# Optimization experiments

Hardware: AMD Instinct MI355X
Metric: run time of the kernel (lower is better)

## Reference

```python
import jax, jax.numpy as jnp
import numpy as np

B, K, LQ, LR, H = 32, 8, 128, 256, 512  # H = hidden_dim*2
L = LQ + K * LR


def setup_inputs() -> dict:
    key = jax.random.key(0)
    ks = jax.random.split(key, 10)
    w = 0.02
    return {
        "h_q": jax.random.normal(ks[0], (B, LQ, H), jnp.float32),
        "q_mask": jnp.ones((B, LQ), jnp.float32),
        "h_r": jax.random.normal(ks[1], (B, K, LR, H), jnp.float32),
        "r_mask": jnp.ones((B, K, LR), jnp.float32),
        "s_t": jax.random.normal(ks[2], (B, H), jnp.float32),
        "qr_cov": jnp.zeros((B, L), jnp.float32),
        # Linear weights stored torch-style [out, in]
        "U_w": jax.random.normal(ks[3], (H, H), jnp.float32) * w,
        "Wc_w": jax.random.normal(ks[4], (H, 1), jnp.float32) * w,
        "Ws_w": jax.random.normal(ks[5], (H, H), jnp.float32) * w,
        "Wqr_w": jax.random.normal(ks[6], (H, H), jnp.float32) * w,
        "Wqr_b": jax.random.normal(ks[7], (H,), jnp.float32) * w,
        "Vr_w": jax.random.normal(ks[8], (1, H), jnp.float32) * w,
    }


def reference(h_q, q_mask, h_r, r_mask, s_t, qr_cov,
              U_w, Wc_w, Ws_w, Wqr_w, Wqr_b, Vr_w):
    b, l_q, h = h_q.shape
    _, k, l_r, _ = h_r.shape

    _h_q = jnp.broadcast_to(h_q[:, None], (b, k, l_q, h)).reshape(b * k, l_q, h)
    _h_r = h_r.reshape(b * k, l_r, h)
    _q_mask = jnp.broadcast_to(q_mask[:, None], (b, k, l_q)).reshape(b * k, l_q)
    _r_mask = r_mask.reshape(b * k, l_r)

    # bilinear co-attention scores: tanh((hq @ U^T) @ hr^T)  [b*k, l_q, l_r]
    hqU = jnp.einsum('bqi,oi->bqo', _h_q, U_w)
    U = jnp.tanh(jnp.einsum('bqo,bro->bqr', hqU, _h_r))

    alpha_q = jax.nn.softmax(jnp.max(U, axis=2), axis=-1)  # [b*k, l_q]
    alpha_r = jax.nn.softmax(jnp.max(U, axis=1), axis=-1)  # [b*k, l_r]

    pai_q = ((alpha_q * _q_mask)[..., None] * _h_q).reshape(b, k, l_q, h).mean(axis=1)
    pai_r = ((alpha_r * _r_mask)[..., None] * _h_r).reshape(b, k * l_r, h)
    qr = jnp.concatenate([pai_q, pai_r], axis=1)  # [b, L, h]

    dec_fea = (jnp.einsum('bi,oi->bo', s_t, Ws_w)[:, None, :]
               + jnp.einsum('bli,oi->blo', qr, Wqr_w) + Wqr_b
               + qr_cov[:, :, None] * Wc_w[:, 0])  # coverage feature

    logits = jnp.einsum('blo,o->bl', jnp.tanh(dec_fea), Vr_w[0])  # [b, L]
    mask = jnp.concatenate([q_mask, r_mask.reshape(b, k * l_r)], axis=1)
    a = jax.nn.softmax(logits, axis=1) * mask
    a = a / jnp.sum(a, axis=1, keepdims=True)

    c_t = jnp.einsum('bl,blh->bh', a, qr)
    new_cov = qr_cov + a
    return (c_t, a, new_cov)
```

## Files before the change

kernel.cpp:

```cpp
#include <hip/hip_runtime.h>
#include <stdint.h>

#define B  32
#define KK 8
#define LQ 128
#define LR 256
#define H  512
#define LL 2176

typedef short s16x8 __attribute__((ext_vector_type(8)));
typedef float f32x4 __attribute__((ext_vector_type(4)));

__device__ __forceinline__ unsigned short f2bf(float f) {
    unsigned int u = __float_as_uint(f);
    unsigned int r = (u + 0x7FFFu + ((u >> 16) & 1u)) >> 16;
    return (unsigned short)r;
}
__device__ __forceinline__ void gload16(const unsigned short* g, unsigned short* l) {
    __builtin_amdgcn_global_load_lds(
        (const __attribute__((address_space(1))) void*)g,
        (__attribute__((address_space(3))) void*)l, 16, 0, 0);
}
__device__ __forceinline__ float fexp2(float x) {
#if __has_builtin(__builtin_amdgcn_exp2f)
    return __builtin_amdgcn_exp2f(x);
#else
    return __expf(x * 0.69314718056f);
#endif
}
__device__ __forceinline__ float frcp(float x) {
#if __has_builtin(__builtin_amdgcn_rcpf)
    return __builtin_amdgcn_rcpf(x);
#else
    return 1.f / x;
#endif
}
__device__ __forceinline__ float fast_tanh(float x) {
    float e = fexp2(x * 2.885390082f);
    return 1.f - 2.f * frcp(1.f + e);
}
#define LOG2E 1.4426950408889634f

#define NQ4 (B * LQ * H / 4)
#define NR4 (B * KK * LR * H / 4)
#define NW4 (H * H / 4)
#define NL4 (B * LL / 4)
#define NC4 (B * H / 4)
#define NWB4 (B * LL / 4)
#define QBLK 256
#define RBLK 4096
#define WBLK 64
#define ZBLK 19
#define SBLK 256
#define K0GRID (QBLK + RBLK + WBLK + ZBLK + SBLK)
__global__ __launch_bounds__(256) void k0_convert(
    const float* __restrict__ h_q, const float* __restrict__ h_r,
    const float* __restrict__ U_w, const float* __restrict__ Wqr_w,
    unsigned short* __restrict__ Xb, unsigned short* __restrict__ Uwb,
    unsigned short* __restrict__ Wqrb, float* __restrict__ logits,
    float* __restrict__ out_ct, float* __restrict__ wbuf,
    const float* __restrict__ s_t, const float* __restrict__ Ws_w,
    float* __restrict__ sWs) {
    int t = threadIdx.x;
    int blk = blockIdx.x;
    ushort4* Xb4 = (ushort4*)Xb;
    if (blk < QBLK + RBLK) {
        const float4* src; ushort4* dst;
        if (blk < QBLK) {
            unsigned u0 = (unsigned)blk * 2048u;
            unsigned b = (unsigned)blk >> 3;
            src = (const float4*)h_q + u0;
            dst = Xb4 + b * 278528u + (u0 & 16383u);
        } else {
            unsigned rb = (unsigned)(blk - QBLK);
            unsigned u0 = rb * 2048u;
            unsigned b = rb >> 7;
            src = (const float4*)h_r + u0;
            dst = Xb4 + b * 278528u + 16384u + (u0 & 262143u);
        }
        float4 v[8];
#pragma unroll
        for (int j = 0; j < 8; ++j) v[j] = src[t + j * 256];
#pragma unroll
        for (int j = 0; j < 8; ++j) {
            ushort4 o;
            o.x = f2bf(v[j].x); o.y = f2bf(v[j].y);
            o.z = f2bf(v[j].z); o.w = f2bf(v[j].w);
            dst[t + j * 256] = o;
        }
    } else if (blk < QBLK + RBLK + WBLK) {
        int wb = blk - (QBLK + RBLK);
        const float4* src = ((wb < 32) ? (const float4*)U_w : (const float4*)Wqr_w)
                            + (unsigned)(wb & 31) * 2048u;
        ushort4* dst = ((wb < 32) ? (ushort4*)Uwb : (ushort4*)Wqrb)
                       + (unsigned)(wb & 31) * 2048u;
        float4 v[8];
#pragma unroll
        for (int j = 0; j < 8; ++j) v[j] = src[t + j * 256];
#pragma unroll
        for (int j = 0; j < 8; ++j) {
            ushort4 o;
            o.x = f2bf(v[j].x); o.y = f2bf(v[j].y);
            o.z = f2bf(v[j].z); o.w = f2bf(v[j].w);
            dst[t + j * 256] = o;
        }
    } else if (blk < QBLK + RBLK + WBLK + ZBLK) {
        unsigned zb = (unsigned)(blk - (QBLK + RBLK + WBLK));
        float4 zero = {0.f, 0.f, 0.f, 0.f};
        float4* lg4 = (float4*)logits;
        float4* ct4 = (float4*)out_ct;
        float4* wb4 = (float4*)wbuf;
#pragma unroll
        for (int j = 0; j < 8; ++j) {
            unsigned z = zb * 2048u + (unsigned)j * 256u + (unsigned)t;
            if (z < NL4) lg4[z] = zero;
            else if (z < NL4 + NC4) ct4[z - NL4] = zero;
            else if (z < NL4 + NC4 + NWB4) wb4[z - NL4 - NC4] = zero;
        }
    } else {
        int idx = blk - (QBLK + RBLK + WBLK + ZBLK);
        int b = idx >> 3, oc = idx & 7;
        __shared__ __align__(16) float sl[H];
        for (int i = t; i < H; i += 256) sl[i] = s_t[b * H + i];
        __syncthreads();
        int o = oc * 64 + (t >> 2);
        int part = t & 3;
        const float4* sl4 = (const float4*)sl;
        const float4* wr4 = (const float4*)(Ws_w + (size_t)o * H);
        float a = 0.f;
#pragma unroll
        for (int ii = 0; ii < 32; ++ii) {
            int i = part + 4 * ii;
            float4 x = sl4[i], y = wr4[i];
            a += x.x * y.x + x.y * y.y + x.z * y.z + x.w * y.w;
        }
        a += __shfl_xor(a, 1);
        a += __shfl_xor(a, 2);
        if (part == 0) sWs[b * H + o] = a;
    }
}

__global__ __launch_bounds__(256) void k1_gemm_hqU(
    const unsigned short* __restrict__ Xb, const unsigned short* __restrict__ Uwb,
    unsigned short* __restrict__ hqU) {
    __shared__ __align__(16) unsigned short As[64 * 64];
    __shared__ __align__(16) unsigned short Bs[128 * 64];
    int tid = threadIdx.x;
    int wave = tid >> 6, lane = tid & 63;
    int quad = lane >> 4, l16 = lane & 15;
    int wr = wave >> 1, wc = wave & 1;
    int g = blockIdx.x;
    int tle = (g & 7) * 32 + (g >> 3);
    int mt = tle >> 2, nt = tle & 3;
    int m0 = mt * 64, n0 = nt * 128;

    const unsigned short* ag[2]; unsigned short* la[2];
    const unsigned short* bg[4]; unsigned short* lb[4];
#pragma unroll
    for (int i = 0; i < 2; ++i) {
        int gg = (wave * 2 + i) * 64 + lane;
        int r = gg >> 3, c = gg & 7, cs = c ^ (r & 7);
        int am = m0 + r;
        ag[i] = Xb + ((size_t)(am >> 7) * LL + (am & 127)) * H + cs * 8;
        la[i] = As + (wave * 2 + i) * 512;
    }
#pragma unroll
    for (int i = 0; i < 4; ++i) {
        int gg = (wave * 4 + i) * 64 + lane;
        int r = gg >> 3, c = gg & 7, cs = c ^ (r & 7);
        bg[i] = Uwb + (size_t)(n0 + r) * H + cs * 8;
        lb[i] = Bs + (wave * 4 + i) * 512;
    }

    f32x4 acc[2][4] = {};
    for (int k0 = 0; k0 < H; k0 += 64) {
#pragma unroll
        for (int i = 0; i < 2; ++i) gload16(ag[i] + k0, la[i]);
#pragma unroll
        for (int i = 0; i < 4; ++i) gload16(bg[i] + k0, lb[i]);
        __syncthreads();
#pragma unroll
        for (int kh = 0; kh < 2; ++kh) {
            s16x8 af[2], bfr[4];
#pragma unroll
            for (int mi = 0; mi < 2; ++mi) {
                int row = wr * 32 + mi * 16 + l16;
                int ch = (kh * 4 + quad) ^ (row & 7);
                af[mi] = *(const s16x8*)&As[(row * 8 + ch) * 8];
            }
#pragma unroll
            for (int ni = 0; ni < 4; ++ni) {
                int row = wc * 64 + ni * 16 + l16;
                int ch = (kh * 4 + quad) ^ (row & 7);
                bfr[ni] = *(const s16x8*)&Bs[(row * 8 + ch) * 8];
            }
#pragma unroll
            for (int mi = 0; mi < 2; ++mi)
#pragma unroll
                for (int ni = 0; ni < 4; ++ni)
                    acc[mi][ni] = __builtin_amdgcn_mfma_f32_16x16x32_bf16(
                        af[mi], bfr[ni], acc[mi][ni], 0, 0, 0);
        }
        __syncthreads();
    }
#pragma unroll
    for (int mi = 0; mi < 2; ++mi)
#pragma unroll
        for (int ni = 0; ni < 4; ++ni)
#pragma unroll
            for (int i = 0; i < 4; ++i) {
                int row = m0 + wr * 32 + mi * 16 + quad * 4 + i;
                int col = n0 + wc * 64 + ni * 16 + l16;
                hqU[(size_t)row * H + col] = f2bf(acc[mi][ni][i]);
            }
}

__global__ __launch_bounds__(256) void k2_scores(
    const unsigned short* __restrict__ hqU, const unsigned short* __restrict__ Xb,
    float* __restrict__ maxq, float* __restrict__ maxr_part) {
    __shared__ __align__(16) unsigned short As[64 * 64];
    __shared__ __align__(16) unsigned short Bs[256 * 64];
    __shared__ float redA[64 * 2];
    __shared__ float redB[256 * 2];
    int g = blockIdx.x;
    int tle = (g & 7) * 64 + (g >> 3);
    int qt = tle & 1, k = (tle >> 1) & 7, b = tle >> 4;
    int tid = threadIdx.x;
    int wave = tid >> 6, lane = tid & 63;
    int quad = lane >> 4, l16 = lane & 15;
    int wr = wave >> 1, wc = wave & 1;

    const unsigned short* Ab = hqU + (size_t)(b * LQ + qt * 64) * H;
    const unsigned short* Bb = Xb + (size_t)(b * LL + LQ + k * LR) * H;

    const unsigned short* ag[2]; unsigned short* la[2];
    const unsigned short* bg[8]; unsigned short* lb[8];
#pragma unroll
    for (int i = 0; i < 2; ++i) {
        int gg = (wave * 2 + i) * 64 + lane;
        int r = gg >> 3, c = gg & 7, cs = c ^ (r & 7);
        ag[i] = Ab + (size_t)r * H + cs * 8;
        la[i] = As + (wave * 2 + i) * 512;
    }
#pragma unroll
    for (int i = 0; i < 8; ++i) {
        int gg = (wave * 8 + i) * 64 + lane;
        int r = gg >> 3, c = gg & 7, cs = c ^ (r & 7);
        bg[i] = Bb + (size_t)r * H + cs * 8;
        lb[i] = Bs + (wave * 8 + i) * 512;
    }

    f32x4 acc[2][8] = {};
    for (int k0 = 0; k0 < H; k0 += 64) {
#pragma unroll
        for (int i = 0; i < 2; ++i) gload16(ag[i] + k0, la[i]);
#pragma unroll
        for (int i = 0; i < 8; ++i) gload16(bg[i] + k0, lb[i]);
        __syncthreads();
#pragma unroll
        for (int kh = 0; kh < 2; ++kh) {
            s16x8 af[2], bfr[8];
#pragma unroll
            for (int mi = 0; mi < 2; ++mi) {
                int row = wr * 32 + mi * 16 + l16;
                int ch = (kh * 4 + quad) ^ (row & 7);
                af[mi] = *(const s16x8*)&As[(row * 8 + ch) * 8];
            }
#pragma unroll
            for (int ni = 0; ni < 8; ++ni) {
                int row = wc * 128 + ni * 16 + l16;
                int ch = (kh * 4 + quad) ^ (row & 7);
                bfr[ni] = *(const s16x8*)&Bs[(row * 8 + ch) * 8];
            }
#pragma unroll
            for (int mi = 0; mi < 2; ++mi)
#pragma unroll
                for (int ni = 0; ni < 8; ++ni)
                    acc[mi][ni] = __builtin_amdgcn_mfma_f32_16x16x32_bf16(
                        af[mi], bfr[ni], acc[mi][ni], 0, 0, 0);
        }
        __syncthreads();
    }
#pragma unroll
    for (int mi = 0; mi < 2; ++mi)
#pragma unroll
        for (int i = 0; i < 4; ++i) {
            float v = acc[mi][0][i];
#pragma unroll
            for (int ni = 1; ni < 8; ++ni) v = fmaxf(v, acc[mi][ni][i]);
            for (int s = 1; s < 16; s <<= 1) v = fmaxf(v, __shfl_xor(v, s));
            if (l16 == 0) redA[(wr * 32 + mi * 16 + quad * 4 + i) * 2 + wc] = v;
        }
#pragma unroll
    for (int ni = 0; ni < 8; ++ni) {
        float v = acc[0][ni][0];
#pragma unroll
        for (int mi = 0; mi < 2; ++mi)
#pragma unroll
            for (int i = 0; i < 4; ++i) v = fmaxf(v, acc[mi][ni][i]);
        for (int s = 16; s < 64; s <<= 1) v = fmaxf(v, __shfl_xor(v, s));
        if (quad == 0) redB[(wc * 128 + ni * 16 + l16) * 2 + wr] = v;
    }
    __syncthreads();
    size_t bk = (size_t)(b * KK + k);
    if (tid < 64)
        maxq[bk * 128 + qt * 64 + tid] = fmaxf(redA[tid * 2 + 0], redA[tid * 2 + 1]);
    maxr_part[(bk * 2 + qt) * 256 + tid] = fmaxf(redB[tid * 2 + 0], redB[tid * 2 + 1]);
}

__global__ __launch_bounds__(256) void k3_alphas(
    const float* __restrict__ maxq, const float* __restrict__ maxr_part,
    const float* __restrict__ r_mask, const float* __restrict__ q_mask,
    float* __restrict__ wbuf) {
    int b = blockIdx.x >> 3, k = blockIdx.x & 7;
    int t = threadIdx.x;
    __shared__ float red[256];
    size_t bk = (size_t)(b * KK + k);
    float vq = -1e30f;
    if (t < 128) vq = fast_tanh(maxq[bk * 128 + t]);
    red[t] = vq; __syncthreads();
    for (int s = 128; s > 0; s >>= 1) { if (t < s) red[t] = fmaxf(red[t], red[t + s]); __syncthreads(); }
    float mxq = red[0]; __syncthreads();
    float eq = (t < 128) ? fexp2((vq - mxq) * LOG2E) : 0.f;
    red[t] = eq; __syncthreads();
    for (int s = 128; s > 0; s >>= 1) { if (t < s) red[t] += red[t + s]; __syncthreads(); }
    float invq = 1.f / red[0]; __syncthreads();
    if (t < 128)
        atomicAdd(&wbuf[b * LL + t], q_mask[b * LQ + t] * eq * invq * 0.125f);
    float vr = fast_tanh(fmaxf(maxr_part[(bk * 2 + 0) * 256 + t],
                               maxr_part[(bk * 2 + 1) * 256 + t]));
    red[t] = vr; __syncthreads();
    for (int s = 128; s > 0; s >>= 1) { if (t < s) red[t] = fmaxf(red[t], red[t + s]); __syncthreads(); }
    float mxr = red[0]; __syncthreads();
    float er = fexp2((vr - mxr) * LOG2E);
    red[t] = er; __syncthreads();
    for (int s = 128; s > 0; s >>= 1) { if (t < s) red[t] += red[t + s]; __syncthreads(); }
    float invr = 1.f / red[0];
    wbuf[b * LL + LQ + k * LR + t] = r_mask[bk * LR + t] * er * invr;
}

__global__ __launch_bounds__(256) void k4_gemm_logits(
    const unsigned short* __restrict__ Xb, const unsigned short* __restrict__ Wqrb,
    const float* __restrict__ sWs, const float* __restrict__ Wqr_b,
    const float* __restrict__ Wc_w, const float* __restrict__ Vr_w,
    const float* __restrict__ wbuf, const float* __restrict__ qr_cov,
    float* __restrict__ logits) {
    __shared__ __align__(16) unsigned short As[128 * 64];
    __shared__ __align__(16) unsigned short Bs[128 * 64];
    __shared__ float wrow[128], covrow[128], sWsl[128], biasl[128], wcl[128], vrl[128];
    int tid = threadIdx.x;
    int wave = tid >> 6, lane = tid & 63;
    int quad = lane >> 4, l16 = lane & 15;
    int wr = wave >> 1, wc = wave & 1;
    int g = blockIdx.x;
    int tle = (g & 7) * 272 + (g >> 3);
    int mt = tle >> 2, nt = tle & 3;
    size_t m0 = (size_t)mt * 128;
    int n0 = nt * 128;
    int b = mt / 17;

    if (tid < 128) {
        wrow[tid]   = wbuf[m0 + tid];
        covrow[tid] = qr_cov[m0 + tid];
        sWsl[tid]   = sWs[b * H + n0 + tid];
        biasl[tid]  = Wqr_b[n0 + tid];
        wcl[tid]    = Wc_w[n0 + tid];
        vrl[tid]    = Vr_w[n0 + tid];
    }

    const unsigned short* ag[4]; unsigned short* la[4];
    const unsigned short* bg[4]; unsigned short* lb[4];
#pragma unroll
    for (int i = 0; i < 4; ++i) {
        int gg = (wave * 4 + i) * 64 + lane;
        int r = gg >> 3, c = gg & 7, cs = c ^ (r & 7);
        ag[i] = Xb + (m0 + r) * H + cs * 8;
        bg[i] = Wqrb + (size_t)(n0 + r) * H + cs * 8;
        la[i] = As + (wave * 4 + i) * 512;
        lb[i] = Bs + (wave * 4 + i) * 512;
    }

    f32x4 acc[4][4] = {};
    for (int k0 = 0; k0 < H; k0 += 64) {
#pragma unroll
        for (int i = 0; i < 4; ++i) gload16(ag[i] + k0, la[i]);
#pragma unroll
        for (int i = 0; i < 4; ++i) gload16(bg[i] + k0, lb[i]);
        __syncthreads();
#pragma unroll
        for (int kh = 0; kh < 2; ++kh) {
            s16x8 af[4], bfr[4];
#pragma unroll
            for (int mi = 0; mi < 4; ++mi) {
                int row = wr * 64 + mi * 16 + l16;
                int ch = (kh * 4 + quad) ^ (row & 7);
                af[mi] = *(const s16x8*)&As[(row * 8 + ch) * 8];
            }
#pragma unroll
            for (int ni = 0; ni < 4; ++ni) {
                int row = wc * 64 + ni * 16 + l16;
                int ch = (kh * 4 + quad) ^ (row & 7);
                bfr[ni] = *(const s16x8*)&Bs[(row * 8 + ch) * 8];
            }
#pragma unroll
            for (int mi = 0; mi < 4; ++mi)
#pragma unroll
                for (int ni = 0; ni < 4; ++ni)
                    acc[mi][ni] = __builtin_amdgcn_mfma_f32_16x16x32_bf16(
                        af[mi], bfr[ni], acc[mi][ni], 0, 0, 0);
        }
        __syncthreads();
    }
#pragma unroll
    for (int mi = 0; mi < 4; ++mi)
#pragma unroll
        for (int i = 0; i < 4; ++i) {
            int rl = wr * 64 + mi * 16 + quad * 4 + i;
            float wv = wrow[rl], cv = covrow[rl];
            float lsum = 0.f;
#pragma unroll
            for (int ni = 0; ni < 4; ++ni) {
                int ol = wc * 64 + ni * 16 + l16;
                float dec = sWsl[ol] + wv * acc[mi][ni][i] + biasl[ol] + cv * wcl[ol];
                lsum += vrl[ol] * fast_tanh(dec);
            }
            for (int s = 1; s < 16; s <<= 1) lsum += __shfl_xor(lsum, s);
            if (l16 == 0) atomicAdd(&logits[m0 + rl], lsum);
        }
}

__global__ __launch_bounds__(256) void k5a_softmax(
    const float* __restrict__ logits, const float* __restrict__ q_mask,
    const float* __restrict__ r_mask, const float* __restrict__ qr_cov,
    const float* __restrict__ wbuf, float* __restrict__ out,
    float* __restrict__ coef) {
    int b = blockIdx.x, t = threadIdx.x;
    __shared__ float lg[LL];
    __shared__ float red[256];
    float mx = -1e30f;
    for (int l = t; l < LL; l += 256) {
        float v = logits[b * LL + l];
        lg[l] = v;
        mx = fmaxf(mx, v);
    }
    red[t] = mx; __syncthreads();
    for (int s = 128; s > 0; s >>= 1) { if (t < s) red[t] = fmaxf(red[t], red[t + s]); __syncthreads(); }
    mx = red[0]; __syncthreads();
    float sum = 0.f;
    for (int l = t; l < LL; l += 256) {
        float e = fexp2((lg[l] - mx) * LOG2E);
        float m = (l < LQ) ? q_mask[b * LQ + l] : r_mask[b * (KK * LR) + l - LQ];
        float em = e * m;
        lg[l] = em;
        sum += em;
    }
    red[t] = sum; __syncthreads();
    for (int s = 128; s > 0; s >>= 1) { if (t < s) red[t] += red[t + s]; __syncthreads(); }
    float inv = 1.f / red[0];
    __syncthreads();
    float* aout = out + B * H + (size_t)b * LL;
    float* cov  = out + B * H + (size_t)B * LL + (size_t)b * LL;
    for (int l = t; l < LL; l += 256) {
        float a = lg[l] * inv;
        aout[l] = a;
        cov[l] = qr_cov[b * LL + l] + a;
        coef[b * LL + l] = a * wbuf[b * LL + l];
    }
}

__global__ __launch_bounds__(256) void k5b_ct(
    const unsigned short* __restrict__ Xb, const float* __restrict__ coef,
    float* __restrict__ out) {
    int b = blockIdx.x / 17, chunk = blockIdx.x % 17;
    int t = threadIdx.x;
    int l0 = chunk * 128;
    __shared__ float cl[128];
    __shared__ float red[4][512];
    if (t < 128) cl[t] = coef[b * LL + l0 + t];
    __syncthreads();
    int rr = t >> 6, lane = t & 63, cc = lane * 8;
    float a[8] = {};
    const unsigned short* xp = Xb + ((size_t)b * LL + l0) * H;
    for (int l = rr; l < 128; l += 4) {
        float c = cl[l];
        uint4 u4 = *(const uint4*)(xp + (size_t)l * H + cc);
        a[0] += c * __uint_as_float(u4.x << 16);
        a[1] += c * __uint_as_float(u4.x & 0xffff0000u);
        a[2] += c * __uint_as_float(u4.y << 16);
        a[3] += c * __uint_as_float(u4.y & 0xffff0000u);
        a[4] += c * __uint_as_float(u4.z << 16);
        a[5] += c * __uint_as_float(u4.z & 0xffff0000u);
        a[6] += c * __uint_as_float(u4.w << 16);
        a[7] += c * __uint_as_float(u4.w & 0xffff0000u);
    }
#pragma unroll
    for (int j = 0; j < 8; ++j) red[rr][cc + j] = a[j];
    __syncthreads();
    int col = t * 2;
    float s0 = red[0][col] + red[1][col] + red[2][col] + red[3][col];
    float s1 = red[0][col + 1] + red[1][col + 1] + red[2][col + 1] + red[3][col + 1];
    atomicAdd(&out[b * H + col], s0);
    atomicAdd(&out[b * H + col + 1], s1);
}

extern "C" void kernel_launch(void* const* d_in, const int* in_sizes, int n_in,
                              void* d_out, int out_size, void* d_ws, size_t ws_size,
                              hipStream_t stream) {
    (void)in_sizes; (void)n_in; (void)out_size; (void)ws_size;
    const float* h_q    = (const float*)d_in[0];
    const float* q_mask = (const float*)d_in[1];
    const float* h_r    = (const float*)d_in[2];
    const float* r_mask = (const float*)d_in[3];
    const float* s_t    = (const float*)d_in[4];
    const float* qr_cov = (const float*)d_in[5];
    const float* U_w    = (const float*)d_in[6];
    const float* Wc_w   = (const float*)d_in[7];
    const float* Ws_w   = (const float*)d_in[8];
    const float* Wqr_w  = (const float*)d_in[9];
    const float* Wqr_b  = (const float*)d_in[10];
    const float* Vr_w   = (const float*)d_in[11];
    float* out = (float*)d_out;

    char* p = (char*)d_ws;
    unsigned short* Xb   = (unsigned short*)p; p += (size_t)B * LL * H * 2;
    unsigned short* Uwb  = (unsigned short*)p; p += (size_t)H * H * 2;
    unsigned short* Wqrb = (unsigned short*)p; p += (size_t)H * H * 2;
    unsigned short* hqU  = (unsigned short*)p; p += (size_t)B * LQ * H * 2;
    float* sWs       = (float*)p; p += (size_t)B * H * 4;
    float* maxq      = (float*)p; p += (size_t)B * KK * 128 * 4;
    float* maxr_part = (float*)p; p += (size_t)B * KK * 2 * 256 * 4;
    float* wbuf      = (float*)p; p += (size_t)B * LL * 4;
    float* logits    = (float*)p; p += (size_t)B * LL * 4;
    float* coef      = (float*)p; p += (size_t)B * LL * 4;

    k0_convert<<<K0GRID, 256, 0, stream>>>(h_q, h_r, U_w, Wqr_w, Xb, Uwb, Wqrb,
                                           logits, out, wbuf, s_t, Ws_w, sWs);
    k1_gemm_hqU<<<256, 256, 0, stream>>>(Xb, Uwb, hqU);
    k2_scores<<<512, 256, 0, stream>>>(hqU, Xb, maxq, maxr_part);
    k3_alphas<<<B * KK, 256, 0, stream>>>(maxq, maxr_part, r_mask, q_mask, wbuf);
    k4_gemm_logits<<<2176, 256, 0, stream>>>(
        Xb, Wqrb, sWs, Wqr_b, Wc_w, Vr_w, wbuf, qr_cov, logits);
    k5a_softmax<<<B, 256, 0, stream>>>(logits, q_mask, r_mask, qr_cov, wbuf, out, coef);
    k5b_ct<<<B * (LL / 128), 256, 0, stream>>>(Xb, coef, out);
}
```

Before: 345.3 us.

## Run logits GEMM in FP8 with scaled MFMA and split ct reduction finer

The conversion kernel now also writes FP8 e4m3 copies of the concatenated activations and of Wqr, and the logits GEMM uses the 16x16x128 f8f6f4 scaled MFMA on 128-wide K tiles instead of bf16 MFMA. This halves the GEMM operand bytes and the MFMA count per tile. The cost is an extra ~35MB FP8 write in the convert pass and lower precision in the logits. The c_t reduction kernel also uses 64-row chunks with twice as many blocks, for more parallelism.

After: 360.0 us. +4.2%, slower.

```diff
diff --git a/kernel.cpp b/kernel.cpp
--- a/kernel.cpp
+++ b/kernel.cpp
@@ -1,4 +1,5 @@
 #include <hip/hip_runtime.h>
+#include <hip/hip_fp8.h>
 #include <stdint.h>
 
 #define B  32
@@ -10,13 +11,18 @@
 
 typedef short s16x8 __attribute__((ext_vector_type(8)));
 typedef float f32x4 __attribute__((ext_vector_type(4)));
+typedef int   i32x8 __attribute__((ext_vector_type(8)));
 
 __device__ __forceinline__ unsigned short f2bf(float f) {
     unsigned int u = __float_as_uint(f);
     unsigned int r = (u + 0x7FFFu + ((u >> 16) & 1u)) >> 16;
     return (unsigned short)r;
 }
-__device__ __forceinline__ void gload16(const unsigned short* g, unsigned short* l) {
+__device__ __forceinline__ unsigned char f2fp8(float f) {
+    __hip_fp8_e4m3 v(f);
+    return (unsigned char)v.__x;
+}
+__device__ __forceinline__ void gload16(const void* g, void* l) {
     __builtin_amdgcn_global_load_lds(
         (const __attribute__((address_space(1))) void*)g,
         (__attribute__((address_space(3))) void*)l, 16, 0, 0);
@@ -57,26 +63,30 @@
     const float* __restrict__ h_q, const float* __restrict__ h_r,
     const float* __restrict__ U_w, const float* __restrict__ Wqr_w,
     unsigned short* __restrict__ Xb, unsigned short* __restrict__ Uwb,
-    unsigned short* __restrict__ Wqrb, float* __restrict__ logits,
+    unsigned short* __restrict__ Wqrb, unsigned char* __restrict__ Xb8,
+    unsigned char* __restrict__ Wqrb8, float* __restrict__ logits,
     float* __restrict__ out_ct, float* __restrict__ wbuf,
     const float* __restrict__ s_t, const float* __restrict__ Ws_w,
     float* __restrict__ sWs) {
     int t = threadIdx.x;
     int blk = blockIdx.x;
     ushort4* Xb4 = (ushort4*)Xb;
+    uchar4* Xb84 = (uchar4*)Xb8;
     if (blk < QBLK + RBLK) {
-        const float4* src; ushort4* dst;
+        const float4* src; ushort4* dst; uchar4* dst8;
         if (blk < QBLK) {
             unsigned u0 = (unsigned)blk * 2048u;
             unsigned b = (unsigned)blk >> 3;
+            unsigned off = b * 278528u + (u0 & 16383u);
             src = (const float4*)h_q + u0;
-            dst = Xb4 + b * 278528u + (u0 & 16383u);
+            dst = Xb4 + off; dst8 = Xb84 + off;
         } else {
             unsigned rb = (unsigned)(blk - QBLK);
             unsigned u0 = rb * 2048u;
             unsigned b = rb >> 7;
+            unsigned off = b * 278528u + 16384u + (u0 & 262143u);
             src = (const float4*)h_r + u0;
-            dst = Xb4 + b * 278528u + 16384u + (u0 & 262143u);
+            dst = Xb4 + off; dst8 = Xb84 + off;
         }
         float4 v[8];
 #pragma unroll
@@ -87,13 +97,19 @@
             o.x = f2bf(v[j].x); o.y = f2bf(v[j].y);
             o.z = f2bf(v[j].z); o.w = f2bf(v[j].w);
             dst[t + j * 256] = o;
+            uchar4 o8;
+            o8.x = f2fp8(v[j].x); o8.y = f2fp8(v[j].y);
+            o8.z = f2fp8(v[j].z); o8.w = f2fp8(v[j].w);
+            dst8[t + j * 256] = o8;
         }
     } else if (blk < QBLK + RBLK + WBLK) {
         int wb = blk - (QBLK + RBLK);
-        const float4* src = ((wb < 32) ? (const float4*)U_w : (const float4*)Wqr_w)
+        bool isU = (wb < 32);
+        const float4* src = (isU ? (const float4*)U_w : (const float4*)Wqr_w)
                             + (unsigned)(wb & 31) * 2048u;
-        ushort4* dst = ((wb < 32) ? (ushort4*)Uwb : (ushort4*)Wqrb)
+        ushort4* dst = (isU ? (ushort4*)Uwb : (ushort4*)Wqrb)
                        + (unsigned)(wb & 31) * 2048u;
+        uchar4* dst8 = (uchar4*)Wqrb8 + (unsigned)(wb & 31) * 2048u;
         float4 v[8];
 #pragma unroll
         for (int j = 0; j < 8; ++j) v[j] = src[t + j * 256];
@@ -103,6 +119,12 @@
             o.x = f2bf(v[j].x); o.y = f2bf(v[j].y);
             o.z = f2bf(v[j].z); o.w = f2bf(v[j].w);
             dst[t + j * 256] = o;
+            if (!isU) {
+                uchar4 o8;
+                o8.x = f2fp8(v[j].x); o8.y = f2fp8(v[j].y);
+                o8.z = f2fp8(v[j].z); o8.w = f2fp8(v[j].w);
+                dst8[t + j * 256] = o8;
+            }
         }
     } else if (blk < QBLK + RBLK + WBLK + ZBLK) {
         unsigned zb = (unsigned)(blk - (QBLK + RBLK + WBLK));
@@ -340,13 +362,13 @@
 }
 
 __global__ __launch_bounds__(256) void k4_gemm_logits(
-    const unsigned short* __restrict__ Xb, const unsigned short* __restrict__ Wqrb,
+    const unsigned char* __restrict__ Xb8, const unsigned char* __restrict__ Wqrb8,
     const float* __restrict__ sWs, const float* __restrict__ Wqr_b,
     const float* __restrict__ Wc_w, const float* __restrict__ Vr_w,
     const float* __restrict__ wbuf, const float* __restrict__ qr_cov,
     float* __restrict__ logits) {
-    __shared__ __align__(16) unsigned short As[128 * 64];
-    __shared__ __align__(16) unsigned short Bs[128 * 64];
+    __shared__ __align__(16) unsigned char As[128 * 128];
+    __shared__ __align__(16) unsigned char Bs[128 * 128];
     __shared__ float wrow[128], covrow[128], sWsl[128], biasl[128], wcl[128], vrl[128];
     int tid = threadIdx.x;
     int wave = tid >> 6, lane = tid & 63;
@@ -368,46 +390,51 @@
         vrl[tid]    = Vr_w[n0 + tid];
     }
 
-    const unsigned short* ag[4]; unsigned short* la[4];
-    const unsigned short* bg[4]; unsigned short* lb[4];
+    const unsigned char* ag[4]; unsigned char* la[4];
+    const unsigned char* bg[4]; unsigned char* lb[4];
 #pragma unroll
     for (int i = 0; i < 4; ++i) {
         int gg = (wave * 4 + i) * 64 + lane;
         int r = gg >> 3, c = gg & 7, cs = c ^ (r & 7);
-        ag[i] = Xb + (m0 + r) * H + cs * 8;
-        bg[i] = Wqrb + (size_t)(n0 + r) * H + cs * 8;
-        la[i] = As + (wave * 4 + i) * 512;
-        lb[i] = Bs + (wave * 4 + i) * 512;
+        ag[i] = Xb8 + (m0 + r) * H + cs * 16;
+        bg[i] = Wqrb8 + (size_t)(n0 + r) * H + cs * 16;
+        la[i] = As + (wave * 4 + i) * 1024;
+        lb[i] = Bs + (wave * 4 + i) * 1024;
     }
 
     f32x4 acc[4][4] = {};
-    for (int k0 = 0; k0 < H; k0 += 64) {
+    for (int k0 = 0; k0 < H; k0 += 128) {
 #pragma unroll
         for (int i = 0; i < 4; ++i) gload16(ag[i] + k0, la[i]);
 #pragma unroll
         for (int i = 0; i < 4; ++i) gload16(bg[i] + k0, lb[i]);
         __syncthreads();
-#pragma unroll
-        for (int kh = 0; kh < 2; ++kh) {
-            s16x8 af[4], bfr[4];
-#pragma unroll
-            for (int mi = 0; mi < 4; ++mi) {
-                int row = wr * 64 + mi * 16 + l16;
-                int ch = (kh * 4 + quad) ^ (row & 7);
-                af[mi] = *(const s16x8*)&As[(row * 8 + ch) * 8];
-            }
-#pragma unroll
-            for (int ni = 0; ni < 4; ++ni) {
-                int row = wc * 64 + ni * 16 + l16;
-                int ch = (kh * 4 + quad) ^ (row & 7);
-                bfr[ni] = *(const s16x8*)&Bs[(row * 8 + ch) * 8];
-            }
+        i32x8 af[4];
+#pragma unroll
+        for (int mi = 0; mi < 4; ++mi) {
+            int row = wr * 64 + mi * 16 + l16;
+            int xs = row & 7;
+            const uint4* rp = (const uint4*)(As + row * 128);
+            uint4 lo = rp[(quad * 2) ^ xs];
+            uint4 hi = rp[(quad * 2 + 1) ^ xs];
+            af[mi][0] = lo.x; af[mi][1] = lo.y; af[mi][2] = lo.z; af[mi][3] = lo.w;
+            af[mi][4] = hi.x; af[mi][5] = hi.y; af[mi][6] = hi.z; af[mi][7] = hi.w;
+        }
+#pragma unroll
+        for (int ni = 0; ni < 4; ++ni) {
+            int row = wc * 64 + ni * 16 + l16;
+            int xs = row & 7;
+            const uint4* rp = (const uint4*)(Bs + row * 128);
+            uint4 lo = rp[(quad * 2) ^ xs];
+            uint4 hi = rp[(quad * 2 + 1) ^ xs];
+            i32x8 bfr;
+            bfr[0] = lo.x; bfr[1] = lo.y; bfr[2] = lo.z; bfr[3] = lo.w;
+            bfr[4] = hi.x; bfr[5] = hi.y; bfr[6] = hi.z; bfr[7] = hi.w;
 #pragma unroll
             for (int mi = 0; mi < 4; ++mi)
-#pragma unroll
-                for (int ni = 0; ni < 4; ++ni)
-                    acc[mi][ni] = __builtin_amdgcn_mfma_f32_16x16x32_bf16(
-                        af[mi], bfr[ni], acc[mi][ni], 0, 0, 0);
+                acc[mi][ni] = __builtin_amdgcn_mfma_scale_f32_16x16x128_f8f6f4(
+                    af[mi], bfr, acc[mi][ni], 0, 0,
+                    0, 0x7F7F7F7F, 0, 0x7F7F7F7F);
         }
         __syncthreads();
     }
@@ -471,17 +498,17 @@
 __global__ __launch_bounds__(256) void k5b_ct(
     const unsigned short* __restrict__ Xb, const float* __restrict__ coef,
     float* __restrict__ out) {
-    int b = blockIdx.x / 17, chunk = blockIdx.x % 17;
+    int b = blockIdx.x / 34, chunk = blockIdx.x % 34;
     int t = threadIdx.x;
-    int l0 = chunk * 128;
-    __shared__ float cl[128];
+    int l0 = chunk * 64;
+    __shared__ float cl[64];
     __shared__ float red[4][512];
-    if (t < 128) cl[t] = coef[b * LL + l0 + t];
+    if (t < 64) cl[t] = coef[b * LL + l0 + t];
     __syncthreads();
     int rr = t >> 6, lane = t & 63, cc = lane * 8;
     float a[8] = {};
     const unsigned short* xp = Xb + ((size_t)b * LL + l0) * H;
-    for (int l = rr; l < 128; l += 4) {
+    for (int l = rr; l < 64; l += 4) {
         float c = cl[l];
         uint4 u4 = *(const uint4*)(xp + (size_t)l * H + cc);
         a[0] += c * __uint_as_float(u4.x << 16);
@@ -522,10 +549,12 @@
     float* out = (float*)d_out;
 
     char* p = (char*)d_ws;
-    unsigned short* Xb   = (unsigned short*)p; p += (size_t)B * LL * H * 2;
-    unsigned short* Uwb  = (unsigned short*)p; p += (size_t)H * H * 2;
-    unsigned short* Wqrb = (unsigned short*)p; p += (size_t)H * H * 2;
-    unsigned short* hqU  = (unsigned short*)p; p += (size_t)B * LQ * H * 2;
+    unsigned short* Xb    = (unsigned short*)p; p += (size_t)B * LL * H * 2;
+    unsigned char*  Xb8   = (unsigned char*)p;  p += (size_t)B * LL * H;
+    unsigned short* Uwb   = (unsigned short*)p; p += (size_t)H * H * 2;
+    unsigned short* Wqrb  = (unsigned short*)p; p += (size_t)H * H * 2;
+    unsigned char*  Wqrb8 = (unsigned char*)p;  p += (size_t)H * H;
+    unsigned short* hqU   = (unsigned short*)p; p += (size_t)B * LQ * H * 2;
     float* sWs       = (float*)p; p += (size_t)B * H * 4;
     float* maxq      = (float*)p; p += (size_t)B * KK * 128 * 4;
     float* maxr_part = (float*)p; p += (size_t)B * KK * 2 * 256 * 4;
@@ -534,12 +563,13 @@
     float* coef      = (float*)p; p += (size_t)B * LL * 4;
 
     k0_convert<<<K0GRID, 256, 0, stream>>>(h_q, h_r, U_w, Wqr_w, Xb, Uwb, Wqrb,
-                                           logits, out, wbuf, s_t, Ws_w, sWs);
+                                           Xb8, Wqrb8, logits, out, wbuf,
+                                           s_t, Ws_w, sWs);
     k1_gemm_hqU<<<256, 256, 0, stream>>>(Xb, Uwb, hqU);
     k2_scores<<<512, 256, 0, stream>>>(hqU, Xb, maxq, maxr_part);
     k3_alphas<<<B * KK, 256, 0, stream>>>(maxq, maxr_part, r_mask, q_mask, wbuf);
     k4_gemm_logits<<<2176, 256, 0, stream>>>(
-        Xb, Wqrb, sWs, Wqr_b, Wc_w, Vr_w, wbuf, qr_cov, logits);
+        Xb8, Wqrb8, sWs, Wqr_b, Wc_w, Vr_w, wbuf, qr_cov, logits);
     k5a_softmax<<<B, 256, 0, stream>>>(logits, q_mask, r_mask, qr_cov, wbuf, out, coef);
-    k5b_ct<<<B * (LL / 128), 256, 0, stream>>>(Xb, coef, out);
-}
+    k5b_ct<<<B * 34, 256, 0, stream>>>(Xb, coef, out);
+}
```
